# Kernel optimization log

Measured on AMD Instinct MI355X. Metric: run time of the kernel, lower is better.

## Reference

```python
import jax, jax.numpy as jnp
import numpy as np

HIDDEN = 768
NUM_BLOCKS = 8
BLOCK = HIDDEN // NUM_BLOCKS
BASE_THR, K_DECAY, MIN_THR = 0.01, 20.0, 0.0005


def _threshold(height, width):
    # wavenumber-dependent soft-shrink threshold T(k), shape [H, W//2+1]
    fu = jnp.fft.fftfreq(height, d=1.0).astype(jnp.float32)[:, None]
    fv = jnp.fft.rfftfreq(width, d=1.0).astype(jnp.float32)[None, :]
    k = jnp.sqrt(fu ** 2 + fv ** 2) * max(height, width)
    thr = BASE_THR * jnp.exp(-0.5 * (k / K_DECAY) ** 2)
    return jnp.maximum(thr, MIN_THR)


def setup_inputs() -> dict:
    key = jax.random.key(0)
    kx, k1, k2, k3, k4 = jax.random.split(key, 5)
    scale = 0.02
    x = jax.random.normal(kx, (4, 128, 128, HIDDEN), dtype=jnp.float32)
    w1 = scale * jax.random.normal(k1, (2, NUM_BLOCKS, BLOCK, BLOCK), dtype=jnp.float32)
    b1 = scale * jax.random.normal(k2, (2, NUM_BLOCKS, BLOCK), dtype=jnp.float32)
    w2 = scale * jax.random.normal(k3, (2, NUM_BLOCKS, BLOCK, BLOCK), dtype=jnp.float32)
    b2 = scale * jax.random.normal(k4, (2, NUM_BLOCKS, BLOCK), dtype=jnp.float32)
    return {"x": x, "w1": w1, "b1": b1, "w2": w2, "b2": b2}


def reference(x, w1, b1, w2, b2):
    dtype = x.dtype
    bias = x
    xf = x.astype(jnp.float32)
    B, H, W, C = xf.shape
    Wc = W // 2 + 1
    # rfft2 over spatial dims, orthonormal
    Xc = jnp.fft.rfft2(xf, axes=(1, 2), norm='ortho')
    Xc = Xc.reshape(B, H, Wc, NUM_BLOCKS, BLOCK)
    xr, xi = jnp.real(Xc), jnp.imag(Xc)
    mm = lambda t, w: jnp.einsum('bhwni,nio->bhwno', t, w)
    # complex block-diagonal 2-layer MLP
    o1r = jax.nn.relu(mm(xr, w1[0]) - mm(xi, w1[1]) + b1[0])
    o1i = jax.nn.relu(mm(xi, w1[0]) + mm(xr, w1[1]) + b1[1])
    o2r = mm(o1r, w2[0]) - mm(o1i, w2[1]) + b2[0]
    o2i = mm(o1i, w2[0]) + mm(o1r, w2[1]) + b2[1]
    # soft-shrink on complex magnitude with wavenumber-dependent threshold
    mag = jnp.sqrt(o2r ** 2 + o2i ** 2 + 1e-8)
    thr = _threshold(H, W)[None, :, :, None, None]  # [1,H,Wc,1,1]
    sf = jax.nn.relu(mag - thr) / mag
    Yc = (o2r * sf) + 1j * (o2i * sf)
    Yc = Yc.reshape(B, H, Wc, C)
    y = jnp.fft.irfft2(Yc, s=(H, W), axes=(1, 2), norm='ortho')
    return y.astype(dtype) + bias
```

## Files before the change

kernel.cpp:

```cpp
#include <hip/hip_runtime.h>
#include <hip/hip_bf16.h>
#include <math.h>


#define HD   768
#define NBLK 8
#define HH   128
#define WW   128
#define WC   65
#define NPOS (HH * WC)

constexpr float SC    = 0.08838834764831845f;
constexpr float TWOPI = 6.28318530717958647692f;

constexpr int TM_OFF     = 0;
constexpr int TW_OFF     = 49152;
constexpr int TWI_OFF    = 69632;
constexpr int WF_OFF     = 90112;
constexpr int WF_END_U16 = 679936;
constexpr size_t A_UINTS = (size_t)4 * NPOS * HD;

typedef __attribute__((ext_vector_type(8))) short short8;
typedef __attribute__((ext_vector_type(4))) float f32x4;

#define MFMA __builtin_amdgcn_mfma_f32_16x16x32_bf16

static __device__ inline unsigned short f2bf(float f) {
  __hip_bfloat16 h = __float2bfloat16(f);
  return __builtin_bit_cast(unsigned short, h);
}
static __device__ inline unsigned int pack2(float re, float im) {
  return (unsigned int)f2bf(re) | ((unsigned int)f2bf(im) << 16);
}
static __device__ inline float lo2f(unsigned int u) {
  return __builtin_bit_cast(float, u << 16);
}
static __device__ inline float hi2f(unsigned int u) {
  return __builtin_bit_cast(float, u & 0xffff0000u);
}

__global__ __launch_bounds__(256) void k_prep(const float* __restrict__ w1,
                                              const float* __restrict__ b1,
                                              const float* __restrict__ w2,
                                              const float* __restrict__ b2,
                                              unsigned short* __restrict__ wf,
                                              float* __restrict__ bpk) {
  const int blk = blockIdx.x, t = threadIdx.x;
  if (blk < 16) {
    const int layer = blk >> 3, n = blk & 7;
    const float* w  = layer ? w2 : w1;
    const float* bs = layer ? b2 : b1;
    unsigned short* dst = wf + WF_OFF + (size_t)blk * (72 * 512);
    for (int e = t; e < 72 * 512; e += 256) {
      int f = e >> 9, idx = e & 511;
      int kk = f / 12, nt = f - kk * 12;
      int lane = idx >> 3, j = idx & 7;
      int k  = kk * 32 + (lane >> 4) * 8 + j;
      int cc = nt * 16 + (lane & 15);
      float v;
      if (k < 96) v = (cc < 96) ? w[(size_t)n * 9216 + k * 96 + cc]
                                : w[(size_t)(8 + n) * 9216 + k * 96 + (cc - 96)];
      else        v = (cc < 96) ? -w[(size_t)(8 + n) * 9216 + (k - 96) * 96 + cc]
                                :  w[(size_t)n * 9216 + (k - 96) * 96 + (cc - 96)];
      dst[e] = f2bf(v);
    }
    for (int c = t; c < 192; c += 256)
      bpk[blk * 192 + c] = (c < 96) ? bs[n * 96 + c] : bs[(8 + n) * 96 + (c - 96)];
  } else if (blk == 16) {
    for (int e = t; e < 96 * 512; e += 256) {
      int f = e >> 9, idx = e & 511;
      int part = f >> 5, rem = f & 31, kot = rem >> 2, kk = rem & 3;
      int lane = idx >> 3, j = idx & 7;
      int ko = kot * 16 + (lane & 15);
      int r  = kk * 32 + (lane >> 4) * 8 + j;
      float sn, cs; sincosf((TWOPI / 128.f) * (float)((ko * r) & 127), &sn, &cs);
      float v = (part == 0) ? cs : (part == 1) ? sn : -sn;
      wf[TM_OFF + (size_t)f * 512 + idx] = f2bf(v * SC);
    }
  } else if (blk == 17) {
    for (int e = t; e < 40 * 512; e += 256) {
      int f = e >> 9, idx = e & 511;
      int mt = f >> 2, kk = f & 3;
      int lane = idx >> 3, j = idx & 7;
      int row = mt * 16 + (lane & 15);
      int r   = kk * 32 + (lane >> 4) * 8 + j;
      int kor = (row < 80) ? row : row - 80;
      float sn, cs; sincosf((TWOPI / 128.f) * (float)((kor * r) & 127), &sn, &cs);
      wf[TW_OFF + (size_t)f * 512 + idx] = f2bf((row < 80 ? cs : -sn) * SC);
    }
  } else {
    for (int e = t; e < 40 * 512; e += 256) {
      int f = e >> 9, idx = e & 511;
      int mt = f / 5, kk = f - mt * 5;
      int lane = idx >> 3, j = idx & 7;
      int wr = mt * 16 + (lane & 15);
      int k  = kk * 32 + (lane >> 4) * 8 + j;
      float v = 0.f;
      if (k < 80) {
        int kb = k;
        if (kb <= 64) {
          float sn, cs; sincosf((TWOPI / 128.f) * (float)((wr * kb) & 127), &sn, &cs);
          v = SC * ((kb == 0 || kb == 64) ? 1.f : 2.f) * cs;
        }
      } else {
        int kb = k - 80;
        if (kb >= 1 && kb <= 63) {
          float sn, cs; sincosf((TWOPI / 128.f) * (float)((wr * kb) & 127), &sn, &cs);
          v = -2.f * SC * sn;
        }
      }
      wf[TWI_OFF + (size_t)f * 512 + idx] = f2bf(v);
    }
  }
}

__global__ __launch_bounds__(256) void k_fft_w(const float* __restrict__ x,
                                               unsigned int* __restrict__ A,
                                               const unsigned short* __restrict__ wf) {
  __shared__ unsigned short Xt[64 * 136];
  const int h = blockIdx.x, c0 = blockIdx.y * 64, b = blockIdx.z, t = threadIdx.x;
  const int wv = t >> 6, lane = t & 63, l15 = lane & 15, lg = lane >> 4;
  const float* xp = x + ((size_t)(b * HH + h)) * WW * HD + c0;
  for (int idx = t; idx < 128 * 64; idx += 256) {
    int r = idx >> 6, ch = idx & 63;
    Xt[ch * 136 + r] = f2bf(xp[(size_t)r * HD + ch]);
  }
  __syncthreads();
  const unsigned short* tw = wf + TW_OFF;
  f32x4 acc[10];
#pragma unroll
  for (int m = 0; m < 10; ++m) acc[m] = { 0.f, 0.f, 0.f, 0.f };
#pragma unroll
  for (int kk = 0; kk < 4; ++kk) {
    short8 bq = *(const short8*)&Xt[(wv * 16 + l15) * 136 + kk * 32 + lg * 8];
#pragma unroll
    for (int m = 0; m < 10; ++m) {
      short8 a = *(const short8*)&tw[(size_t)(m * 4 + kk) * 512 + lane * 8];
      acc[m] = MFMA(a, bq, acc[m], 0, 0, 0);
    }
  }
  unsigned int* Ao = A + ((size_t)b * NPOS + h * WC) * HD + c0 + wv * 16 + l15;
#pragma unroll
  for (int q = 0; q < 5; ++q)
#pragma unroll
    for (int r = 0; r < 4; ++r) {
      int ko = q * 16 + lg * 4 + r;
      if (ko <= 64) Ao[(size_t)ko * HD] = pack2(acc[q][r], acc[5 + q][r]);
    }
}

__global__ __launch_bounds__(256) void k_ifft_w(const unsigned int* __restrict__ A,
                                                const unsigned int* __restrict__ Bp,
                                                float* __restrict__ out,
                                                const unsigned short* __restrict__ wf) {
  __shared__ unsigned short Zt[64 * 168];
  const int h = blockIdx.x, c0 = blockIdx.y * 64, b = blockIdx.z, t = threadIdx.x;
  const int wv = t >> 6, lane = t & 63, l15 = lane & 15, lg = lane >> 4;
  const size_t base = ((size_t)b * NPOS + h * WC) * HD + c0;
  for (int idx = t; idx < 65 * 64; idx += 256) {
    int kb = idx >> 6, ch = idx & 63;
    unsigned int uA = A[base + (size_t)kb * HD + ch];
    unsigned int uB = Bp[base + (size_t)kb * HD + ch];
    float re = lo2f(uA) + lo2f(uB);
    float im = hi2f(uA) + hi2f(uB);
    Zt[ch * 168 + kb]      = f2bf(re);
    Zt[ch * 168 + 80 + kb] = (kb == 0 || kb == 64) ? (unsigned short)0 : f2bf(im);
  }
  for (int idx = t; idx < 64 * 32; idx += 256) {
    int ch = idx >> 5, q = idx & 31;
    if (q < 30) {
      int kb = 65 + (q % 15), half = q / 15;
      Zt[ch * 168 + half * 80 + kb] = 0;
    }
  }
  __syncthreads();
  const unsigned short* twi = wf + TWI_OFF;
  f32x4 acc[8];
#pragma unroll
  for (int m = 0; m < 8; ++m) acc[m] = { 0.f, 0.f, 0.f, 0.f };
#pragma unroll
  for (int kk = 0; kk < 5; ++kk) {
    short8 bq = *(const short8*)&Zt[(wv * 16 + l15) * 168 + kk * 32 + lg * 8];
#pragma unroll
    for (int m = 0; m < 8; ++m) {
      short8 a = *(const short8*)&twi[(size_t)(m * 5 + kk) * 512 + lane * 8];
      acc[m] = MFMA(a, bq, acc[m], 0, 0, 0);
    }
  }
#pragma unroll
  for (int m = 0; m < 8; ++m)
#pragma unroll
    for (int r = 0; r < 4; ++r) {
      int wr = m * 16 + lg * 4 + r;
      size_t go = (((size_t)(b * HH + h)) * WW + wr) * HD + c0 + wv * 16 + l15;
      out[go] = acc[m][r];
    }
}

template <int FWD>
static __device__ inline void dft_gemm16(const unsigned short* Rb, const unsigned short* Ib,
                                         const unsigned short* tm, int rt, int cb, int lane,
                                         f32x4* aR, f32x4* aI) {
  const int l15 = lane & 15, lg = lane >> 4;
#pragma unroll
  for (int kkr = 0; kkr < 4; ++kkr) {
    const int r0 = kkr * 32 + lg * 8;
    short8 Ac = *(const short8*)&tm[(size_t)(0 * 32 + rt * 4 + kkr) * 512 + lane * 8];
    short8 As = *(const short8*)&tm[(size_t)(1 * 32 + rt * 4 + kkr) * 512 + lane * 8];
    short8 An = *(const short8*)&tm[(size_t)(2 * 32 + rt * 4 + kkr) * 512 + lane * 8];
#pragma unroll
    for (int c = 0; c < 3; ++c) {
      short8 zr = *(const short8*)&Rb[((cb + c) * 16 + l15) * 136 + r0];
      short8 zi = *(const short8*)&Ib[((cb + c) * 16 + l15) * 136 + r0];
      aR[c] = MFMA(Ac, zr, aR[c], 0, 0, 0);
      if constexpr (FWD) {
        aR[c] = MFMA(As, zi, aR[c], 0, 0, 0);
        aI[c] = MFMA(Ac, zi, aI[c], 0, 0, 0);
        aI[c] = MFMA(An, zr, aI[c], 0, 0, 0);
      } else {
        aR[c] = MFMA(An, zi, aR[c], 0, 0, 0);
        aI[c] = MFMA(Ac, zi, aI[c], 0, 0, 0);
        aI[c] = MFMA(As, zr, aI[c], 0, 0, 0);
      }
    }
  }
}

__global__ __launch_bounds__(1024) void k_mid(const unsigned int* __restrict__ A,
                                              unsigned int* __restrict__ Bp,
                                              const unsigned short* __restrict__ wf,
                                              const float* __restrict__ bpk) {
  __shared__ unsigned short Rb[13312], Ib[13312];
  __shared__ unsigned short WfX[2][12 * 512];
  const int kv = blockIdx.x, n = blockIdx.y, b = blockIdx.z, t = threadIdx.x;
  const int w = t >> 6, lane = t & 63, l15 = lane & 15, lg = lane >> 4;
  const int rt = w >> 1, cb = (w & 1) * 3;
  const size_t pbase = ((size_t)b * NPOS + kv) * HD + n * 96;
  const unsigned short* tm = wf + TM_OFF;
  const unsigned short* wf1 = wf + WF_OFF + (size_t)n * (72 * 512);
  const unsigned short* wf2 = wf + WF_OFF + (size_t)(8 + n) * (72 * 512);

  for (int idx = t; idx < 128 * 96; idx += 1024) {
    int r = idx / 96, ch = idx - r * 96;
    unsigned int u = A[pbase + (size_t)r * (WC * HD) + ch];
    Rb[ch * 136 + r] = (unsigned short)(u & 0xffffu);
    Ib[ch * 136 + r] = (unsigned short)(u >> 16);
  }
  if (t < 768) ((int4*)WfX[0])[t] = ((const int4*)(wf1 + 0 * 12 * 512))[t];
  __syncthreads();

  f32x4 aR[3], aI[3];
#pragma unroll
  for (int c = 0; c < 3; ++c) { aR[c] = {0.f,0.f,0.f,0.f}; aI[c] = {0.f,0.f,0.f,0.f}; }
  dft_gemm16<1>(Rb, Ib, tm, rt, cb, lane, aR, aI);
  if (t < 768) ((int4*)WfX[1])[t] = ((const int4*)(wf1 + 1 * 12 * 512))[t];
  __syncthreads();

#pragma unroll
  for (int c = 0; c < 3; ++c)
#pragma unroll
    for (int r = 0; r < 4; ++r) {
      int row = rt * 16 + lg * 4 + r, ch = (cb + c) * 16 + l15;
      Rb[row * 104 + ch] = f2bf(aR[c][r]);
      Ib[row * 104 + ch] = f2bf(aI[c][r]);
    }
  __syncthreads();

  const int row_a = (rt * 16 + l15) * 104;
  f32x4 acc[6];
#pragma unroll
  for (int i = 0; i < 3; ++i) {
    float bv = bpk[n * 192 + (cb + i) * 16 + l15];
    acc[i] = { bv, bv, bv, bv };
    bv = bpk[n * 192 + (cb + i + 6) * 16 + l15];
    acc[3 + i] = { bv, bv, bv, bv };
  }

#define MLP_PAIR(k0, BUF)                                                        \
  {                                                                              \
    short8 aRf = *(const short8*)&Rb[row_a + (k0) * 32 + lg * 8];                \
    short8 aIf = *(const short8*)&Ib[row_a + (k0) * 32 + lg * 8];                \
    _Pragma("unroll")                                                            \
    for (int i = 0; i < 6; ++i) {                                                \
      int nt = cb + (i < 3 ? i : i + 3);                                         \
      short8 b0 = *(const short8*)&(BUF)[nt * 512 + lane * 8];                   \
      acc[i] = MFMA(aRf, b0, acc[i], 0, 0, 0);                                   \
      int nt2 = (nt < 6) ? nt + 6 : nt - 6;                                      \
      int4 nb = *(const int4*)&(BUF)[nt2 * 512 + lane * 8];                      \
      if (nt < 6) { nb.x ^= 0x80008000; nb.y ^= 0x80008000;                      \
                    nb.z ^= 0x80008000; nb.w ^= 0x80008000; }                    \
      acc[i] = MFMA(aIf, __builtin_bit_cast(short8, nb), acc[i], 0, 0, 0);       \
    }                                                                            \
  }

  MLP_PAIR(0, WfX[0]);
  __syncthreads();
  MLP_PAIR(1, WfX[1]);
  if (t < 768) ((int4*)WfX[0])[t] = ((const int4*)(wf1 + 2 * 12 * 512))[t];
  __syncthreads();
  MLP_PAIR(2, WfX[0]);
  if (t < 768) ((int4*)WfX[1])[t] = ((const int4*)(wf2 + 0 * 12 * 512))[t];
  __syncthreads();

#pragma unroll
  for (int i = 0; i < 3; ++i)
#pragma unroll
    for (int r = 0; r < 4; ++r) {
      int row = rt * 16 + lg * 4 + r, ch = (cb + i) * 16 + l15;
      Rb[row * 104 + ch] = f2bf(fmaxf(acc[i][r], 0.f));
      Ib[row * 104 + ch] = f2bf(fmaxf(acc[3 + i][r], 0.f));
    }
  if (t < 768) ((int4*)WfX[0])[t] = ((const int4*)(wf2 + 1 * 12 * 512))[t];
  __syncthreads();

#pragma unroll
  for (int i = 0; i < 3; ++i) {
    float bv = bpk[(8 + n) * 192 + (cb + i) * 16 + l15];
    acc[i] = { bv, bv, bv, bv };
    bv = bpk[(8 + n) * 192 + (cb + i + 6) * 16 + l15];
    acc[3 + i] = { bv, bv, bv, bv };
  }
  MLP_PAIR(0, WfX[1]);
  __syncthreads();
  MLP_PAIR(1, WfX[0]);
  if (t < 768) ((int4*)WfX[1])[t] = ((const int4*)(wf2 + 2 * 12 * 512))[t];
  __syncthreads();
  MLP_PAIR(2, WfX[1]);
  __syncthreads();

#pragma unroll
  for (int r = 0; r < 4; ++r) {
    int ko = rt * 16 + lg * 4 + r;
    float kus = (ko >= 64) ? (float)(ko - 128) : (float)ko;
    float k2v = kus * kus + (float)(kv * kv);
    float thr = fmaxf(0.01f * expf(-0.00125f * k2v), 0.0005f);
#pragma unroll
    for (int i = 0; i < 3; ++i) {
      float mr = acc[i][r], mi = acc[3 + i][r];
      float mag = sqrtf(mr * mr + mi * mi + 1e-8f);
      float sf = fmaxf(mag - thr, 0.f) / mag;
      int ch = (cb + i) * 16 + l15;
      Rb[ch * 136 + ko] = f2bf(mr * sf);
      Ib[ch * 136 + ko] = f2bf(mi * sf);
    }
  }
  __syncthreads();

#pragma unroll
  for (int c = 0; c < 3; ++c) { aR[c] = {0.f,0.f,0.f,0.f}; aI[c] = {0.f,0.f,0.f,0.f}; }
  dft_gemm16<0>(Rb, Ib, tm, rt, cb, lane, aR, aI);
#pragma unroll
  for (int c = 0; c < 3; ++c)
#pragma unroll
    for (int r = 0; r < 4; ++r) {
      int rr = rt * 16 + lg * 4 + r, ch = (cb + c) * 16 + l15;
      Bp[pbase + (size_t)rr * (WC * HD) + ch] = pack2(aR[c][r], aI[c][r]);
    }
#undef MLP_PAIR
}

extern "C" void kernel_launch(void* const* d_in, const int* in_sizes, int n_in,
                              void* d_out, int out_size, void* d_ws, size_t ws_size,
                              hipStream_t stream) {
  const float* x  = (const float*)d_in[0];
  const float* w1 = (const float*)d_in[1];
  const float* b1 = (const float*)d_in[2];
  const float* w2 = (const float*)d_in[3];
  const float* b2 = (const float*)d_in[4];
  float* out = (float*)d_out;
  unsigned int* A  = (unsigned int*)d_ws;
  unsigned int* Bp = A + A_UINTS;

  unsigned short* wf = (unsigned short*)(Bp + A_UINTS);
  float* bpk = (float*)(wf + WF_END_U16);

  k_prep<<<19, 256, 0, stream>>>(w1, b1, w2, b2, wf, bpk);
  k_fft_w<<<dim3(HH, HD / 64, 4), 256, 0, stream>>>(x, A, wf);
  k_mid<<<dim3(WC, NBLK, 4), 1024, 0, stream>>>(A, Bp, wf, bpk);
  k_ifft_w<<<dim3(HH, HD / 64, 4), 256, 0, stream>>>(A, Bp, out, wf);
}
```

Baseline: 405.1 us.

## Stage full per-layer MLP weights in LDS instead of double-buffered chunks

k_mid now loads each layer's whole 72-tile weight set into one large LDS buffer, rather than streaming 12-tile chunks through two ping-pong buffers. Each layer runs as a single 6×6 MFMA loop over the real and imaginary K-halves. This drops the intermediate __syncthreads between chunks and the sign-flip XOR on the imaginary weight tiles, which presumes the prepacked weights already hold the negated tiles. In exchange LDS use per block grows to roughly 127 KB, which likely permits only one 1024-thread block per CU. The weight loads also no longer overlap with MFMA work.

```diff
diff --git a/kernel.cpp b/kernel.cpp
--- a/kernel.cpp
+++ b/kernel.cpp
@@ -231,7 +231,7 @@
                                               const unsigned short* __restrict__ wf,
                                               const float* __restrict__ bpk) {
   __shared__ unsigned short Rb[13312], Ib[13312];
-  __shared__ unsigned short WfX[2][12 * 512];
+  __shared__ unsigned short WfL[72 * 512];
   const int kv = blockIdx.x, n = blockIdx.y, b = blockIdx.z, t = threadIdx.x;
   const int w = t >> 6, lane = t & 63, l15 = lane & 15, lg = lane >> 4;
   const int rt = w >> 1, cb = (w & 1) * 3;
@@ -246,14 +246,14 @@
     Rb[ch * 136 + r] = (unsigned short)(u & 0xffffu);
     Ib[ch * 136 + r] = (unsigned short)(u >> 16);
   }
-  if (t < 768) ((int4*)WfX[0])[t] = ((const int4*)(wf1 + 0 * 12 * 512))[t];
+  for (int idx = t; idx < 4608; idx += 1024)
+    ((int4*)WfL)[idx] = ((const int4*)wf1)[idx];
   __syncthreads();
 
   f32x4 aR[3], aI[3];
 #pragma unroll
   for (int c = 0; c < 3; ++c) { aR[c] = {0.f,0.f,0.f,0.f}; aI[c] = {0.f,0.f,0.f,0.f}; }
   dft_gemm16<1>(Rb, Ib, tm, rt, cb, lane, aR, aI);
-  if (t < 768) ((int4*)WfX[1])[t] = ((const int4*)(wf1 + 1 * 12 * 512))[t];
   __syncthreads();
 
 #pragma unroll
@@ -276,30 +276,20 @@
     acc[3 + i] = { bv, bv, bv, bv };
   }
 
-#define MLP_PAIR(k0, BUF)                                                        \
-  {                                                                              \
-    short8 aRf = *(const short8*)&Rb[row_a + (k0) * 32 + lg * 8];                \
-    short8 aIf = *(const short8*)&Ib[row_a + (k0) * 32 + lg * 8];                \
+#define MLP_LAYER()                                                              \
+  _Pragma("unroll")                                                              \
+  for (int kk = 0; kk < 6; ++kk) {                                               \
+    short8 af = (kk < 3) ? *(const short8*)&Rb[row_a + kk * 32 + lg * 8]         \
+                         : *(const short8*)&Ib[row_a + (kk - 3) * 32 + lg * 8];  \
     _Pragma("unroll")                                                            \
     for (int i = 0; i < 6; ++i) {                                                \
       int nt = cb + (i < 3 ? i : i + 3);                                         \
-      short8 b0 = *(const short8*)&(BUF)[nt * 512 + lane * 8];                   \
-      acc[i] = MFMA(aRf, b0, acc[i], 0, 0, 0);                                   \
-      int nt2 = (nt < 6) ? nt + 6 : nt - 6;                                      \
-      int4 nb = *(const int4*)&(BUF)[nt2 * 512 + lane * 8];                      \
-      if (nt < 6) { nb.x ^= 0x80008000; nb.y ^= 0x80008000;                      \
-                    nb.z ^= 0x80008000; nb.w ^= 0x80008000; }                    \
-      acc[i] = MFMA(aIf, __builtin_bit_cast(short8, nb), acc[i], 0, 0, 0);       \
+      short8 bf = *(const short8*)&WfL[(kk * 12 + nt) * 512 + lane * 8];         \
+      acc[i] = MFMA(af, bf, acc[i], 0, 0, 0);                                    \
     }                                                                            \
   }
 
-  MLP_PAIR(0, WfX[0]);
-  __syncthreads();
-  MLP_PAIR(1, WfX[1]);
-  if (t < 768) ((int4*)WfX[0])[t] = ((const int4*)(wf1 + 2 * 12 * 512))[t];
-  __syncthreads();
-  MLP_PAIR(2, WfX[0]);
-  if (t < 768) ((int4*)WfX[1])[t] = ((const int4*)(wf2 + 0 * 12 * 512))[t];
+  MLP_LAYER();
   __syncthreads();
 
 #pragma unroll
@@ -310,7 +300,8 @@
       Rb[row * 104 + ch] = f2bf(fmaxf(acc[i][r], 0.f));
       Ib[row * 104 + ch] = f2bf(fmaxf(acc[3 + i][r], 0.f));
     }
-  if (t < 768) ((int4*)WfX[0])[t] = ((const int4*)(wf2 + 1 * 12 * 512))[t];
+  for (int idx = t; idx < 4608; idx += 1024)
+    ((int4*)WfL)[idx] = ((const int4*)wf2)[idx];
   __syncthreads();
 
 #pragma unroll
@@ -320,12 +311,7 @@
     bv = bpk[(8 + n) * 192 + (cb + i + 6) * 16 + l15];
     acc[3 + i] = { bv, bv, bv, bv };
   }
-  MLP_PAIR(0, WfX[1]);
-  __syncthreads();
-  MLP_PAIR(1, WfX[0]);
-  if (t < 768) ((int4*)WfX[1])[t] = ((const int4*)(wf2 + 2 * 12 * 512))[t];
-  __syncthreads();
-  MLP_PAIR(2, WfX[1]);
+  MLP_LAYER();
   __syncthreads();
 
 #pragma unroll
@@ -356,7 +342,7 @@
       int rr = rt * 16 + lg * 4 + r, ch = (cb + c) * 16 + l15;
       Bp[pbase + (size_t)rr * (WC * HD) + ch] = pack2(aR[c][r], aI[c][r]);
     }
-#undef MLP_PAIR
+#undef MLP_LAYER
 }
 
 extern "C" void kernel_launch(void* const* d_in, const int* in_sizes, int n_in,
```

Result: slower. 419.9 us (+3.7%).

## Halve k_mid block to 8 waves, each owning a full 16-row tile across all channels

Applied to the files above, without the earlier changes.

k_mid now runs 512 threads (8 waves) per block instead of 1024. Each wave handles one 16-row strip across all 96 channels, and all 12 output tiles in the MLP. Previously, pairs of waves split the channels. The change means each wave reuses its A-fragments (DFT matrix rows and activation rows) across twice as many MFMAs, and it removes some barriers, because a wave's rows are no longer shared with another wave between stages. The cost is more accumulator registers per wave (12 f32x4 plus 12 for the DFT) and half as many waves to hide latency, with the same LDS footprint per block.

```diff
diff --git a/kernel.cpp b/kernel.cpp
--- a/kernel.cpp
+++ b/kernel.cpp
@@ -198,20 +198,20 @@
 }
 
 template <int FWD>
-static __device__ inline void dft_gemm16(const unsigned short* Rb, const unsigned short* Ib,
-                                         const unsigned short* tm, int rt, int cb, int lane,
-                                         f32x4* aR, f32x4* aI) {
+static __device__ inline void dft_gemm8(const unsigned short* Rb, const unsigned short* Ib,
+                                        const unsigned short* tm, int w, int lane,
+                                        f32x4* aR, f32x4* aI) {
   const int l15 = lane & 15, lg = lane >> 4;
 #pragma unroll
   for (int kkr = 0; kkr < 4; ++kkr) {
     const int r0 = kkr * 32 + lg * 8;
-    short8 Ac = *(const short8*)&tm[(size_t)(0 * 32 + rt * 4 + kkr) * 512 + lane * 8];
-    short8 As = *(const short8*)&tm[(size_t)(1 * 32 + rt * 4 + kkr) * 512 + lane * 8];
-    short8 An = *(const short8*)&tm[(size_t)(2 * 32 + rt * 4 + kkr) * 512 + lane * 8];
-#pragma unroll
-    for (int c = 0; c < 3; ++c) {
-      short8 zr = *(const short8*)&Rb[((cb + c) * 16 + l15) * 136 + r0];
-      short8 zi = *(const short8*)&Ib[((cb + c) * 16 + l15) * 136 + r0];
+    short8 Ac = *(const short8*)&tm[(size_t)(0 * 32 + w * 4 + kkr) * 512 + lane * 8];
+    short8 As = *(const short8*)&tm[(size_t)(1 * 32 + w * 4 + kkr) * 512 + lane * 8];
+    short8 An = *(const short8*)&tm[(size_t)(2 * 32 + w * 4 + kkr) * 512 + lane * 8];
+#pragma unroll
+    for (int c = 0; c < 6; ++c) {
+      short8 zr = *(const short8*)&Rb[(c * 16 + l15) * 136 + r0];
+      short8 zi = *(const short8*)&Ib[(c * 16 + l15) * 136 + r0];
       aR[c] = MFMA(Ac, zr, aR[c], 0, 0, 0);
       if constexpr (FWD) {
         aR[c] = MFMA(As, zi, aR[c], 0, 0, 0);
@@ -226,120 +226,116 @@
   }
 }
 
-__global__ __launch_bounds__(1024) void k_mid(const unsigned int* __restrict__ A,
-                                              unsigned int* __restrict__ Bp,
-                                              const unsigned short* __restrict__ wf,
-                                              const float* __restrict__ bpk) {
+__global__ __launch_bounds__(512) void k_mid(const unsigned int* __restrict__ A,
+                                             unsigned int* __restrict__ Bp,
+                                             const unsigned short* __restrict__ wf,
+                                             const float* __restrict__ bpk) {
   __shared__ unsigned short Rb[13312], Ib[13312];
   __shared__ unsigned short WfX[2][12 * 512];
   const int kv = blockIdx.x, n = blockIdx.y, b = blockIdx.z, t = threadIdx.x;
   const int w = t >> 6, lane = t & 63, l15 = lane & 15, lg = lane >> 4;
-  const int rt = w >> 1, cb = (w & 1) * 3;
   const size_t pbase = ((size_t)b * NPOS + kv) * HD + n * 96;
   const unsigned short* tm = wf + TM_OFF;
   const unsigned short* wf1 = wf + WF_OFF + (size_t)n * (72 * 512);
   const unsigned short* wf2 = wf + WF_OFF + (size_t)(8 + n) * (72 * 512);
 
-  for (int idx = t; idx < 128 * 96; idx += 1024) {
+#define LOAD_X(BUFI, SRC, KP)                                                    \
+  for (int idx = t; idx < 768; idx += 512)                                       \
+    ((int4*)WfX[BUFI])[idx] = ((const int4*)((SRC) + (KP) * 12 * 512))[idx];
+
+  for (int idx = t; idx < 128 * 96; idx += 512) {
     int r = idx / 96, ch = idx - r * 96;
     unsigned int u = A[pbase + (size_t)r * (WC * HD) + ch];
     Rb[ch * 136 + r] = (unsigned short)(u & 0xffffu);
     Ib[ch * 136 + r] = (unsigned short)(u >> 16);
   }
-  if (t < 768) ((int4*)WfX[0])[t] = ((const int4*)(wf1 + 0 * 12 * 512))[t];
-  __syncthreads();
-
-  f32x4 aR[3], aI[3];
-#pragma unroll
-  for (int c = 0; c < 3; ++c) { aR[c] = {0.f,0.f,0.f,0.f}; aI[c] = {0.f,0.f,0.f,0.f}; }
-  dft_gemm16<1>(Rb, Ib, tm, rt, cb, lane, aR, aI);
-  if (t < 768) ((int4*)WfX[1])[t] = ((const int4*)(wf1 + 1 * 12 * 512))[t];
-  __syncthreads();
-
-#pragma unroll
-  for (int c = 0; c < 3; ++c)
-#pragma unroll
-    for (int r = 0; r < 4; ++r) {
-      int row = rt * 16 + lg * 4 + r, ch = (cb + c) * 16 + l15;
+  LOAD_X(0, wf1, 0);
+  __syncthreads();
+
+  f32x4 aR[6], aI[6];
+#pragma unroll
+  for (int c = 0; c < 6; ++c) { aR[c] = {0.f,0.f,0.f,0.f}; aI[c] = {0.f,0.f,0.f,0.f}; }
+  dft_gemm8<1>(Rb, Ib, tm, w, lane, aR, aI);
+  LOAD_X(1, wf1, 1);
+  __syncthreads();
+
+#pragma unroll
+  for (int c = 0; c < 6; ++c)
+#pragma unroll
+    for (int r = 0; r < 4; ++r) {
+      int row = w * 16 + lg * 4 + r, ch = c * 16 + l15;
       Rb[row * 104 + ch] = f2bf(aR[c][r]);
       Ib[row * 104 + ch] = f2bf(aI[c][r]);
     }
-  __syncthreads();
-
-  const int row_a = (rt * 16 + l15) * 104;
-  f32x4 acc[6];
-#pragma unroll
-  for (int i = 0; i < 3; ++i) {
-    float bv = bpk[n * 192 + (cb + i) * 16 + l15];
-    acc[i] = { bv, bv, bv, bv };
-    bv = bpk[n * 192 + (cb + i + 6) * 16 + l15];
-    acc[3 + i] = { bv, bv, bv, bv };
-  }
-
-#define MLP_PAIR(k0, BUF)                                                        \
+
+  const int row_a = (w * 16 + l15) * 104;
+  f32x4 acc[12];
+#pragma unroll
+  for (int nt = 0; nt < 12; ++nt) {
+    float bv = bpk[n * 192 + nt * 16 + l15];
+    acc[nt] = { bv, bv, bv, bv };
+  }
+
+#define MLP_PAIR(BUF)                                                            \
   {                                                                              \
-    short8 aRf = *(const short8*)&Rb[row_a + (k0) * 32 + lg * 8];                \
-    short8 aIf = *(const short8*)&Ib[row_a + (k0) * 32 + lg * 8];                \
+    short8 aRf = *(const short8*)&Rb[row_a + PK * 32 + lg * 8];                  \
+    short8 aIf = *(const short8*)&Ib[row_a + PK * 32 + lg * 8];                  \
     _Pragma("unroll")                                                            \
-    for (int i = 0; i < 6; ++i) {                                                \
-      int nt = cb + (i < 3 ? i : i + 3);                                         \
+    for (int nt = 0; nt < 12; ++nt) {                                            \
       short8 b0 = *(const short8*)&(BUF)[nt * 512 + lane * 8];                   \
-      acc[i] = MFMA(aRf, b0, acc[i], 0, 0, 0);                                   \
+      acc[nt] = MFMA(aRf, b0, acc[nt], 0, 0, 0);                                 \
       int nt2 = (nt < 6) ? nt + 6 : nt - 6;                                      \
       int4 nb = *(const int4*)&(BUF)[nt2 * 512 + lane * 8];                      \
       if (nt < 6) { nb.x ^= 0x80008000; nb.y ^= 0x80008000;                      \
                     nb.z ^= 0x80008000; nb.w ^= 0x80008000; }                    \
-      acc[i] = MFMA(aIf, __builtin_bit_cast(short8, nb), acc[i], 0, 0, 0);       \
+      acc[nt] = MFMA(aIf, __builtin_bit_cast(short8, nb), acc[nt], 0, 0, 0);     \
     }                                                                            \
   }
 
-  MLP_PAIR(0, WfX[0]);
-  __syncthreads();
-  MLP_PAIR(1, WfX[1]);
-  if (t < 768) ((int4*)WfX[0])[t] = ((const int4*)(wf1 + 2 * 12 * 512))[t];
-  __syncthreads();
-  MLP_PAIR(2, WfX[0]);
-  if (t < 768) ((int4*)WfX[1])[t] = ((const int4*)(wf2 + 0 * 12 * 512))[t];
-  __syncthreads();
-
-#pragma unroll
-  for (int i = 0; i < 3; ++i)
-#pragma unroll
-    for (int r = 0; r < 4; ++r) {
-      int row = rt * 16 + lg * 4 + r, ch = (cb + i) * 16 + l15;
+  { const int PK = 0; MLP_PAIR(WfX[0]); }
+  { const int PK = 1; MLP_PAIR(WfX[1]); }
+  __syncthreads();
+  LOAD_X(0, wf1, 2);
+  LOAD_X(1, wf2, 0);
+  __syncthreads();
+  { const int PK = 2; MLP_PAIR(WfX[0]); }
+
+#pragma unroll
+  for (int i = 0; i < 6; ++i)
+#pragma unroll
+    for (int r = 0; r < 4; ++r) {
+      int row = w * 16 + lg * 4 + r, ch = i * 16 + l15;
       Rb[row * 104 + ch] = f2bf(fmaxf(acc[i][r], 0.f));
-      Ib[row * 104 + ch] = f2bf(fmaxf(acc[3 + i][r], 0.f));
-    }
-  if (t < 768) ((int4*)WfX[0])[t] = ((const int4*)(wf2 + 1 * 12 * 512))[t];
-  __syncthreads();
-
-#pragma unroll
-  for (int i = 0; i < 3; ++i) {
-    float bv = bpk[(8 + n) * 192 + (cb + i) * 16 + l15];
-    acc[i] = { bv, bv, bv, bv };
-    bv = bpk[(8 + n) * 192 + (cb + i + 6) * 16 + l15];
-    acc[3 + i] = { bv, bv, bv, bv };
-  }
-  MLP_PAIR(0, WfX[1]);
-  __syncthreads();
-  MLP_PAIR(1, WfX[0]);
-  if (t < 768) ((int4*)WfX[1])[t] = ((const int4*)(wf2 + 2 * 12 * 512))[t];
-  __syncthreads();
-  MLP_PAIR(2, WfX[1]);
+      Ib[row * 104 + ch] = f2bf(fmaxf(acc[6 + i][r], 0.f));
+    }
+#pragma unroll
+  for (int nt = 0; nt < 12; ++nt) {
+    float bv = bpk[(8 + n) * 192 + nt * 16 + l15];
+    acc[nt] = { bv, bv, bv, bv };
+  }
+  __syncthreads();
+  LOAD_X(0, wf2, 1);
+
+  { const int PK = 0; MLP_PAIR(WfX[1]); }
+  __syncthreads();
+  LOAD_X(1, wf2, 2);
+  { const int PK = 1; MLP_PAIR(WfX[0]); }
+  __syncthreads();
+  { const int PK = 2; MLP_PAIR(WfX[1]); }
   __syncthreads();
 
 #pragma unroll
   for (int r = 0; r < 4; ++r) {
-    int ko = rt * 16 + lg * 4 + r;
+    int ko = w * 16 + lg * 4 + r;
     float kus = (ko >= 64) ? (float)(ko - 128) : (float)ko;
     float k2v = kus * kus + (float)(kv * kv);
     float thr = fmaxf(0.01f * expf(-0.00125f * k2v), 0.0005f);
 #pragma unroll
-    for (int i = 0; i < 3; ++i) {
-      float mr = acc[i][r], mi = acc[3 + i][r];
+    for (int i = 0; i < 6; ++i) {
+      float mr = acc[i][r], mi = acc[6 + i][r];
       float mag = sqrtf(mr * mr + mi * mi + 1e-8f);
       float sf = fmaxf(mag - thr, 0.f) / mag;
-      int ch = (cb + i) * 16 + l15;
+      int ch = i * 16 + l15;
       Rb[ch * 136 + ko] = f2bf(mr * sf);
       Ib[ch * 136 + ko] = f2bf(mi * sf);
     }
@@ -347,16 +343,17 @@
   __syncthreads();
 
 #pragma unroll
-  for (int c = 0; c < 3; ++c) { aR[c] = {0.f,0.f,0.f,0.f}; aI[c] = {0.f,0.f,0.f,0.f}; }
-  dft_gemm16<0>(Rb, Ib, tm, rt, cb, lane, aR, aI);
-#pragma unroll
-  for (int c = 0; c < 3; ++c)
-#pragma unroll
-    for (int r = 0; r < 4; ++r) {
-      int rr = rt * 16 + lg * 4 + r, ch = (cb + c) * 16 + l15;
+  for (int c = 0; c < 6; ++c) { aR[c] = {0.f,0.f,0.f,0.f}; aI[c] = {0.f,0.f,0.f,0.f}; }
+  dft_gemm8<0>(Rb, Ib, tm, w, lane, aR, aI);
+#pragma unroll
+  for (int c = 0; c < 6; ++c)
+#pragma unroll
+    for (int r = 0; r < 4; ++r) {
+      int rr = w * 16 + lg * 4 + r, ch = c * 16 + l15;
       Bp[pbase + (size_t)rr * (WC * HD) + ch] = pack2(aR[c][r], aI[c][r]);
     }
 #undef MLP_PAIR
+#undef LOAD_X
 }
 
 extern "C" void kernel_launch(void* const* d_in, const int* in_sizes, int n_in,
@@ -376,6 +373,6 @@
 
   k_prep<<<19, 256, 0, stream>>>(w1, b1, w2, b2, wf, bpk);
   k_fft_w<<<dim3(HH, HD / 64, 4), 256, 0, stream>>>(x, A, wf);
-  k_mid<<<dim3(WC, NBLK, 4), 1024, 0, stream>>>(A, Bp, wf, bpk);
+  k_mid<<<dim3(WC, NBLK, 4), 512, 0, stream>>>(A, Bp, wf, bpk);
   k_ifft_w<<<dim3(HH, HD / 64, 4), 256, 0, stream>>>(A, Bp, out, wf);
 }
```

Result: no change. 410.9 us (+1.4%).
